# Kernel tuning notes

Measured on AMD Instinct MI355X. Metric: run time of the kernel, lower is better.

The kernel has to match this reference:

```python
import jax, jax.numpy as jnp
import numpy as np

B, S, D_MODEL = 2, 2048, 2048
H, DS, DG, DV = 16, 64, 64, 128
ROPE_BASE = 10000.0
NEG_INF = -1e9


def _rope(x, base=ROPE_BASE):
    # x: [B, S, H, D] -> rotate-half RoPE over positions 0..S-1
    d = x.shape[-1]
    half = d // 2
    inv_freq = 1.0 / (base ** (jnp.arange(half, dtype=jnp.float32) / half))
    ang = jnp.arange(x.shape[1], dtype=jnp.float32)[:, None] * inv_freq  # [S, half]
    cos = jnp.cos(ang)[None, :, None, :]
    sin = jnp.sin(ang)[None, :, None, :]
    x1, x2 = x[..., :half], x[..., half:]
    return jnp.concatenate([x1 * cos - x2 * sin, x1 * sin + x2 * cos], axis=-1)


def setup_inputs() -> dict:
    key = jax.random.key(0)
    ks = jax.random.split(key, 8)
    s = lambda fan_in: 1.0 / np.sqrt(fan_in)
    return {
        "x": jax.random.normal(ks[0], (B, S, D_MODEL), dtype=jnp.float32),
        "wq_sem": jax.random.normal(ks[1], (D_MODEL, H * DS), dtype=jnp.float32) * s(D_MODEL),
        "wk_sem": jax.random.normal(ks[2], (D_MODEL, H * DS), dtype=jnp.float32) * s(D_MODEL),
        "wq_geo": jax.random.normal(ks[3], (D_MODEL, H * DG), dtype=jnp.float32) * s(D_MODEL),
        "wk_geo": jax.random.normal(ks[4], (D_MODEL, H * DG), dtype=jnp.float32) * s(D_MODEL),
        "wv": jax.random.normal(ks[5], (D_MODEL, H * DV), dtype=jnp.float32) * s(D_MODEL),
        "wo": jax.random.normal(ks[6], (H * DV, D_MODEL), dtype=jnp.float32) * s(H * DV),
        "gate_logit": jax.random.normal(ks[7], (H,), dtype=jnp.float32),
    }


def reference(x, wq_sem, wk_sem, wq_geo, wk_geo, wv, wo, gate_logit):
    b, sl, _ = x.shape
    # Projections -> [B, S, H, d]
    qs = (x @ wq_sem).reshape(b, sl, H, DS)
    ksem = (x @ wk_sem).reshape(b, sl, H, DS)
    qg = _rope((x @ wq_geo).reshape(b, sl, H, DG))
    kg = _rope((x @ wk_geo).reshape(b, sl, H, DG))
    v = (x @ wv).reshape(b, sl, H, DV)

    sem_scale = 1.0 / np.sqrt(DS)
    geo_scale = 1.0 / np.sqrt(DG)
    sem_scores = jnp.einsum("bqhd,bkhd->bhqk", qs, ksem) * sem_scale
    geo_scores = jnp.einsum("bqhd,bkhd->bhqk", qg, kg) * geo_scale

    # Learned per-head gate mixing semantic vs geometric paths
    g = jax.nn.sigmoid(gate_logit)[None, :, None, None]
    scores = g * sem_scores + (1.0 - g) * geo_scores

    causal = jnp.tril(jnp.ones((sl, sl), dtype=bool))
    scores = jnp.where(causal[None, None], scores, NEG_INF)
    attn = jax.nn.softmax(scores, axis=-1)

    out = jnp.einsum("bhqk,bkhd->bqhd", attn, v).reshape(b, sl, H * DV)
    return out @ wo
```

## Files before the change

kernel.cpp:

```cpp
#include <hip/hip_runtime.h>
#include <hip/hip_bf16.h>

typedef unsigned short u16;
typedef __attribute__((ext_vector_type(4))) float floatx4;
typedef __attribute__((ext_vector_type(8))) __bf16 bf16x8;

__device__ __forceinline__ u16 f2bf(float f) {
  unsigned int x = __builtin_bit_cast(unsigned int, f);
  unsigned int r = (x + 0x7fffu + ((x >> 16) & 1u)) >> 16;
  return (u16)r;
}
__device__ __forceinline__ float bf2f(u16 u) {
  unsigned int x = ((unsigned int)u) << 16;
  return __builtin_bit_cast(float, x);
}
__device__ __forceinline__ floatx4 mfma16(bf16x8 a, bf16x8 b, floatx4 c) {
  return __builtin_amdgcn_mfma_f32_16x16x32_bf16(a, b, c, 0, 0, 0);
}
__device__ __forceinline__ void gload16(const u16* g, u16* l) {
  __builtin_amdgcn_global_load_lds(
      (const __attribute__((address_space(1))) unsigned int*)g,
      (__attribute__((address_space(3))) unsigned int*)l, 16, 0, 0);
}
#define SCHEDB() __builtin_amdgcn_sched_barrier(0)
#define SBAR() __builtin_amdgcn_s_barrier()

#define BB 2
#define SS 2048
#define DM 2048
#define HH 16
#define PCOLS 6144

__global__ void convert_bf16_k(const float* __restrict__ src, u16* __restrict__ dst, size_t n) {
  size_t i = ((size_t)blockIdx.x * blockDim.x + threadIdx.x) * 4;
  if (i + 3 >= n) { for (size_t j = i; j < n; ++j) dst[j] = f2bf(src[j]); return; }
  float4 v = *(const float4*)&src[i];
  ushort4 o; o.x = f2bf(v.x); o.y = f2bf(v.y); o.z = f2bf(v.z); o.w = f2bf(v.w);
  *(ushort4*)&dst[i] = o;
}

__global__ void transpose_all_k(const float* w0, const float* w1, const float* w2,
                                const float* w3, const float* w4, const float* w5,
                                u16* __restrict__ WcatT, u16* __restrict__ WoT) {
  __shared__ float tile[32][33];
  const int z = blockIdx.z;
  const float* src; u16* dst; int cols;
  if (z == 0)      { src = w0; dst = WcatT;                        cols = 1024; }
  else if (z == 1) { src = w1; dst = WcatT + (size_t)1024 * 2048;  cols = 1024; }
  else if (z == 2) { src = w2; dst = WcatT + (size_t)2048 * 2048;  cols = 1024; }
  else if (z == 3) { src = w3; dst = WcatT + (size_t)3072 * 2048;  cols = 1024; }
  else if (z == 4) { src = w4; dst = WcatT + (size_t)4096 * 2048;  cols = 2048; }
  else             { src = w5; dst = WoT;                          cols = 2048; }
  int c0 = blockIdx.x * 32;
  if (c0 >= cols) return;
  int r0 = blockIdx.y * 32;
  int tx = threadIdx.x, ty = threadIdx.y;
#pragma unroll
  for (int i = 0; i < 4; ++i)
    tile[ty + i * 8][tx] = src[(size_t)(r0 + ty + i * 8) * cols + c0 + tx];
  __syncthreads();
#pragma unroll
  for (int i = 0; i < 4; ++i)
    dst[(size_t)(c0 + ty + i * 8) * 2048 + r0 + tx] = f2bf(tile[tx][ty + i * 8]);
}

__global__ void vtrans_k(const u16* __restrict__ P, u16* __restrict__ VtG) {
  __shared__ u16 t[32][33];
  int b = blockIdx.z;
  int c0 = blockIdx.x * 32;
  int s0 = blockIdx.y * 32;
  int tx = threadIdx.x, ty = threadIdx.y;
#pragma unroll
  for (int i = 0; i < 4; ++i)
    t[ty + i * 8][tx] = P[((size_t)b * SS + s0 + ty + i * 8) * PCOLS + 4096 + c0 + tx];
  __syncthreads();
#pragma unroll
  for (int i = 0; i < 4; ++i)
    VtG[((size_t)b * 2048 + c0 + ty + i * 8) * SS + s0 + tx] = t[tx][ty + i * 8];
}

__global__ void rope_table_k(float* __restrict__ cosT, float* __restrict__ sinT) {
  int idx = blockIdx.x * 256 + threadIdx.x;
  int s = idx >> 5, d = idx & 31;
  double inv = pow(10000.0, -(double)d / 32.0);
  double ang = (double)s * inv;
  cosT[idx] = (float)cos(ang);
  sinT[idx] = (float)sin(ang);
}

__global__ void rope_apply_k(u16* __restrict__ P, const float* __restrict__ cosT,
                             const float* __restrict__ sinT) {
  int idx = blockIdx.x * 256 + threadIdx.x;
  int d = idx & 31, h = (idx >> 5) & 15, reg = (idx >> 9) & 1, row = idx >> 10;
  int s = row & (SS - 1);
  size_t base = (size_t)row * PCOLS + (reg ? 3072 : 2048) + h * 64 + d;
  float x1 = bf2f(P[base]), x2 = bf2f(P[base + 32]);
  float c = cosT[s * 32 + d], sn = sinT[s * 32 + d];
  P[base] = f2bf(x1 * c - x2 * sn);
  P[base + 32] = f2bf(x1 * sn + x2 * c);
}

template <int NFB, bool OUTF32>
__global__ __launch_bounds__(256, 1)
void gemm4_k(const u16* __restrict__ A, const u16* __restrict__ Bt,
             void* __restrict__ Cout, int M, int N, int K) {
  constexpr int BH = NFB / 2;
  __shared__ alignas(16) u16 lds[16384 + NFB * 8192];
  const int tid = threadIdx.x;
  const int wid = tid >> 6, lane = tid & 63;
  const int lr = lane & 15, lg = lane >> 4;
  const int m0 = blockIdx.y * 128, n0 = blockIdx.x * (NFB * 64);
  const int NT = K >> 6;
  const int NSLAB = NT * 4;

  const int aoff = lr * 32 + ((lg ^ ((lr >> 1) & 3)) * 8);

  const int srow = wid * 16 + (lane >> 2);
  const int sgl = (((lane & 3) ^ ((lane >> 3) & 3)) * 8);
  const u16* Asrc = A + (size_t)(m0 + srow) * K + sgl;
  const u16* Bsrc = Bt + (size_t)(n0 + srow) * K + sgl;

  floatx4 acc[8][NFB];
#pragma unroll
  for (int m = 0; m < 8; ++m)
#pragma unroll
    for (int n = 0; n < NFB; ++n) acc[m][n] = (floatx4){0.f, 0.f, 0.f, 0.f};

  auto stgA = [&](int tile, int kh) {
    u16* d = lds + ((tile & 1) * 2 + kh) * 4096 + wid * 512;
    const u16* s = Asrc + tile * 64 + kh * 32;
#pragma unroll
    for (int c = 0; c < 2; ++c) gload16(s + (size_t)(c * 64) * K, d + c * 2048);
  };
  auto stgB = [&](int tile, int kh) {
    u16* d = lds + 16384 + ((tile & 1) * 2 + kh) * (NFB * 2048) + wid * 512;
    const u16* s = Bsrc + tile * 64 + kh * 32;
#pragma unroll
    for (int c = 0; c < NFB; ++c) gload16(s + (size_t)(c * 64) * K, d + c * 2048);
  };
  auto stage_slab = [&](int s) {
    if (s >= NSLAB) return;
    int tile = s >> 2, kind = s & 3;
    if (kind == 0) stgA(tile, 0);
    else if (kind == 1) stgB(tile, 0);
    else if (kind == 2) stgA(tile, 1);
    else stgB(tile, 1);
  };

  for (int s = 0; s < 7; ++s) stage_slab(s);
  if constexpr (NFB == 6) asm volatile("s_waitcnt vmcnt(10)" ::: "memory");
  else                    asm volatile("s_waitcnt vmcnt(8)" ::: "memory");
  SCHEDB(); SBAR(); SCHEDB();

  bf16x8 af[8], bfv[BH];

#pragma unroll 1
  for (int it = 0; it < (NT >> 1); ++it) {
    const int t = it * 2;
    const int sb = t * 4 + 6;
    const bool more = (t + 2 < NT);

#define PH(BUF, KK, NH, SL, DOVM)                                               \
    {                                                                           \
      const u16* Ab = lds + ((BUF) * 2 + (KK)) * 4096;                          \
      const u16* Bb = lds + 16384 + ((BUF) * 2 + (KK)) * (NFB * 2048);          \
      if ((NH) == 0) {                                                          \
        _Pragma("unroll") for (int m = 0; m < 8; ++m)                           \
          af[m] = *(const bf16x8*)&Ab[(m * 16) * 32 + aoff];                    \
      }                                                                         \
      _Pragma("unroll") for (int j = 0; j < BH; ++j)                            \
        bfv[j] = *(const bf16x8*)&Bb[(wid * NFB * 16 + ((NH) * BH + j) * 16) * 32 + aoff]; \
      stage_slab(sb + (SL));                                                    \
      SCHEDB(); SBAR(); SCHEDB();                                               \
      __builtin_amdgcn_s_setprio(1);                                            \
      _Pragma("unroll") for (int m = 0; m < 8; ++m)                             \
        _Pragma("unroll") for (int j = 0; j < BH; ++j)                          \
          acc[m][(NH) * BH + j] = mfma16(af[m], bfv[j], acc[m][(NH) * BH + j]); \
      __builtin_amdgcn_s_setprio(0);                                            \
      if (DOVM) {                                                               \
        if (more) {                                                             \
          if constexpr (NFB == 6) asm volatile("s_waitcnt vmcnt(10)" ::: "memory"); \
          else                    asm volatile("s_waitcnt vmcnt(8)" ::: "memory");  \
        } else {                                                                \
          asm volatile("s_waitcnt vmcnt(0)" ::: "memory");                      \
        }                                                                       \
      }                                                                         \
      SCHEDB(); SBAR(); SCHEDB();                                               \
    }

    PH(0, 0, 0, 1, 0)
    PH(0, 0, 1, 2, 0)
    PH(0, 1, 0, 3, 0)
    PH(0, 1, 1, 4, 1)
    PH(1, 0, 0, 5, 0)
    PH(1, 0, 1, 6, 0)
    PH(1, 1, 0, 7, 0)
    PH(1, 1, 1, 8, 1)
#undef PH
  }

#pragma unroll
  for (int m = 0; m < 8; ++m) {
    int row0 = m0 + m * 16 + lg * 4;
#pragma unroll
    for (int n = 0; n < NFB; ++n) {
      int col = n0 + wid * NFB * 16 + n * 16 + lr;
#pragma unroll
      for (int r = 0; r < 4; ++r) {
        size_t off = (size_t)(row0 + r) * N + col;
        if (OUTF32) ((float*)Cout)[off] = acc[m][n][r];
        else        ((u16*)Cout)[off] = f2bf(acc[m][n][r]);
      }
    }
  }
}

__device__ __forceinline__ bf16x8 load_scaled(const u16* p, float s) {
  uint4 raw = *(const uint4*)p;
  const u16* ru = (const u16*)&raw;
  bf16x8 out;
#pragma unroll
  for (int j = 0; j < 8; ++j) out[j] = (__bf16)(bf2f(ru[j]) * s);
  return out;
}

__global__ __launch_bounds__(256, 3)
void attn_k(const u16* __restrict__ P, const u16* __restrict__ VtG,
            const float* __restrict__ gate, u16* __restrict__ AttO) {
  const int pairi = blockIdx.x >> 4;
  const int h = blockIdx.x & 15;
  const int b = blockIdx.y;
  const int tid = threadIdx.x, wid = tid >> 6, lane = tid & 63;
  const int lr = lane & 15, lg = lane >> 4;
  const size_t rowb = (size_t)b * SS;

  const float g = 1.f / (1.f + __expf(-gate[h]));
  const float ssc = g * 0.125f;
  const float gsc = (1.f - g) * 0.125f;

  __shared__ alignas(16) u16 Ks[64 * 64];
  __shared__ alignas(16) u16 Kg[64 * 64];
  __shared__ alignas(16) u16 Vt[128 * 64];
  __shared__ alignas(16) u16 Pw[4][16 * 64];

  const int strow = tid >> 3;
  const int stg = ((tid & 7) ^ (strow & 7)) * 8;
  const int swz = lr & 7;

  for (int half = 0; half < 2; ++half) {
    const int qb = half ? (31 - pairi) : pairi;
    const int q0 = qb * 64;

    const u16* qbase = P + (rowb + q0 + wid * 16 + lr) * PCOLS + h * 64;
    bf16x8 qs[2], qg[2];
#pragma unroll
    for (int kk = 0; kk < 2; ++kk) {
      qs[kk] = load_scaled(qbase + kk * 32 + lg * 8, ssc);
      qg[kk] = load_scaled(qbase + 2048 + kk * 32 + lg * 8, gsc);
    }

    float m_r = -1e30f, l_r = 0.f;
    floatx4 o[8];
#pragma unroll
    for (int n = 0; n < 8; ++n) o[n] = (floatx4){0.f, 0.f, 0.f, 0.f};

    const int nkv = q0 + 64;
    for (int kv0 = 0; kv0 < nkv; kv0 += 64) {
      __syncthreads();
      {
        const u16* ks = P + (rowb + kv0 + strow) * PCOLS + 1024 + h * 64 + stg;
        const u16* gs = P + (rowb + kv0 + strow) * PCOLS + 3072 + h * 64 + stg;
        gload16(ks, Ks + wid * 512);
        gload16(gs, Kg + wid * 512);
        gload16(ks + (size_t)32 * PCOLS, Ks + 2048 + wid * 512);
        gload16(gs + (size_t)32 * PCOLS, Kg + 2048 + wid * 512);
      }
      {
        const u16* vs = VtG + ((size_t)b * 2048 + h * 128 + strow) * SS + kv0 + stg;
#pragma unroll
        for (int c = 0; c < 4; ++c)
          gload16(vs + (size_t)(c * 32) * SS, Vt + c * 2048 + wid * 512);
      }
      __syncthreads();

      floatx4 sc[4];
#pragma unroll
      for (int s = 0; s < 4; ++s) sc[s] = (floatx4){0.f, 0.f, 0.f, 0.f};
#pragma unroll
      for (int kk = 0; kk < 2; ++kk) {
#pragma unroll
        for (int s = 0; s < 4; ++s) {
          bf16x8 kf = *(const bf16x8*)&Ks[(s * 16 + lr) * 64 + ((kk * 4 + lg) ^ swz) * 8];
          bf16x8 gf = *(const bf16x8*)&Kg[(s * 16 + lr) * 64 + ((kk * 4 + lg) ^ swz) * 8];
          sc[s] = mfma16(kf, qs[kk], sc[s]);
          sc[s] = mfma16(gf, qg[kk], sc[s]);
        }
      }

      const int qrow = q0 + wid * 16 + lr;
      const bool needmask = (kv0 + 63 > q0 + wid * 16);
      float vv[4][4];
      float vmax = -1e30f;
#pragma unroll
      for (int s = 0; s < 4; ++s)
#pragma unroll
        for (int r = 0; r < 4; ++r) {
          float val = sc[s][r];
          if (needmask) val = (kv0 + s * 16 + lg * 4 + r <= qrow) ? val : -1e30f;
          vv[s][r] = val;
          vmax = fmaxf(vmax, val);
        }
      vmax = fmaxf(vmax, __shfl_xor(vmax, 16));
      vmax = fmaxf(vmax, __shfl_xor(vmax, 32));
      float mnew = fmaxf(m_r, vmax);
      float corr = __expf(m_r - mnew);
      float psum = 0.f;
#pragma unroll
      for (int s = 0; s < 4; ++s)
#pragma unroll
        for (int r = 0; r < 4; ++r) {
          vv[s][r] = __expf(vv[s][r] - mnew);
          psum += vv[s][r];
        }
      psum += __shfl_xor(psum, 16);
      psum += __shfl_xor(psum, 32);
      l_r = l_r * corr + psum;
      m_r = mnew;

#pragma unroll
      for (int s = 0; s < 4; ++s)
#pragma unroll
        for (int t = 0; t < 2; ++t) {
          unsigned int w;
          asm("v_cvt_pk_bf16_f32 %0, %1, %2" : "=v"(w) : "v"(vv[s][2 * t]), "v"(vv[s][2 * t + 1]));
          int u16off = lr * 64 + ((s * 2 + (lg >> 1)) ^ swz) * 8 + (lg & 1) * 4 + t * 2;
          *(unsigned int*)&Pw[wid][u16off] = w;
        }

      float crr[4];
#pragma unroll
      for (int r = 0; r < 4; ++r) crr[r] = __shfl(corr, lg * 4 + r);
#pragma unroll
      for (int n = 0; n < 8; ++n)
#pragma unroll
        for (int r = 0; r < 4; ++r) o[n][r] *= crr[r];

      asm volatile("s_waitcnt lgkmcnt(0)" ::: "memory");
      SCHEDB();
      bf16x8 pa0 = *(const bf16x8*)&Pw[wid][lr * 64 + (lg ^ swz) * 8];
      bf16x8 pa1 = *(const bf16x8*)&Pw[wid][lr * 64 + ((4 + lg) ^ swz) * 8];
#pragma unroll
      for (int n = 0; n < 8; ++n) {
        bf16x8 vb0 = *(const bf16x8*)&Vt[(n * 16 + lr) * 64 + (lg ^ swz) * 8];
        bf16x8 vb1 = *(const bf16x8*)&Vt[(n * 16 + lr) * 64 + ((4 + lg) ^ swz) * 8];
        o[n] = mfma16(pa0, vb0, o[n]);
        o[n] = mfma16(pa1, vb1, o[n]);
      }
    }

    float linv = 1.f / l_r;
    float lnv[4];
#pragma unroll
    for (int r = 0; r < 4; ++r) lnv[r] = __shfl(linv, lg * 4 + r);
#pragma unroll
    for (int n = 0; n < 8; ++n)
#pragma unroll
      for (int r = 0; r < 4; ++r) {
        float val = o[n][r] * lnv[r];
        AttO[(rowb + q0 + wid * 16 + lg * 4 + r) * (size_t)(HH * 128) + h * 128 + n * 16 + lr] =
            f2bf(val);
      }
  }
}

extern "C" void kernel_launch(void* const* d_in, const int* in_sizes, int n_in,
                              void* d_out, int out_size, void* d_ws, size_t ws_size,
                              hipStream_t stream) {
  const float* x       = (const float*)d_in[0];
  const float* wq_sem  = (const float*)d_in[1];
  const float* wk_sem  = (const float*)d_in[2];
  const float* wq_geo  = (const float*)d_in[3];
  const float* wk_geo  = (const float*)d_in[4];
  const float* wv      = (const float*)d_in[5];
  const float* wo      = (const float*)d_in[6];
  const float* gate    = (const float*)d_in[7];

  char* ws = (char*)d_ws;
  u16* Xbf   = (u16*)(ws);
  u16* WcatT = (u16*)(ws + 16777216);
  u16* WoT   = (u16*)(ws + 16777216 + 25165824);
  u16* P     = (u16*)(ws + 16777216 + 25165824 + 8388608);
  float* cosT = (float*)(ws + 16777216 + 25165824 + 8388608 + 50331648);
  float* sinT = cosT + 2048 * 32;
  u16* AttO = Xbf;
  u16* VtG  = WcatT;

  dim3 tb(32, 8);
  convert_bf16_k<<<8192, 256, 0, stream>>>(x, Xbf, (size_t)4096 * 2048);
  transpose_all_k<<<dim3(64, 64, 6), tb, 0, stream>>>(wq_sem, wk_sem, wq_geo, wk_geo,
                                                      wv, wo, WcatT, WoT);
  rope_table_k<<<256, 256, 0, stream>>>(cosT, sinT);

  gemm4_k<6, false><<<dim3(16, 32), 256, 0, stream>>>(Xbf, WcatT, P, 4096, 6144, 2048);
  rope_apply_k<<<16384, 256, 0, stream>>>(P, cosT, sinT);
  vtrans_k<<<dim3(64, 64, 2), tb, 0, stream>>>(P, VtG);
  attn_k<<<dim3(256, 2), 256, 0, stream>>>(P, VtG, gate, AttO);
  gemm4_k<4, true><<<dim3(8, 32), 256, 0, stream>>>(AttO, WoT, d_out, 4096, 2048, 2048);
}
```

Measured before the change: 266.0 us.

## Double-buffer K tiles in LDS and load V directly into registers

The K/Kg tiles are now double-buffered in shared memory, and the next tile is prefetched while the current one is being computed, with explicit vmcnt waits in place of a load-then-sync pattern. The V tile is no longer staged through LDS. Each wave reads its V fragments straight from global memory into registers before the QK work, so the latency is hidden behind the softmax. This trims LDS traffic and one barrier per iteration. In exchange it uses many more VGPRs (16 bf16x8 values), which risks lower occupancy, and each wave makes redundant global reads of V.

```diff
diff --git a/kernel.cpp b/kernel.cpp
--- a/kernel.cpp
+++ b/kernel.cpp
@@ -238,14 +238,15 @@
   const float ssc = g * 0.125f;
   const float gsc = (1.f - g) * 0.125f;
 
-  __shared__ alignas(16) u16 Ks[64 * 64];
-  __shared__ alignas(16) u16 Kg[64 * 64];
-  __shared__ alignas(16) u16 Vt[128 * 64];
+  __shared__ alignas(16) u16 Ks[2][64 * 64];
+  __shared__ alignas(16) u16 Kg[2][64 * 64];
   __shared__ alignas(16) u16 Pw[4][16 * 64];
 
   const int strow = tid >> 3;
   const int stg = ((tid & 7) ^ (strow & 7)) * 8;
   const int swz = lr & 7;
+
+  const u16* vbase0 = VtG + ((size_t)b * 2048 + h * 128 + lr) * SS + lg * 8;
 
   for (int half = 0; half < 2; ++half) {
     const int qb = half ? (31 - pairi) : pairi;
@@ -265,23 +266,35 @@
     for (int n = 0; n < 8; ++n) o[n] = (floatx4){0.f, 0.f, 0.f, 0.f};
 
     const int nkv = q0 + 64;
+
+    auto stageK = [&](int kv0, int buf) {
+      const u16* ks = P + (rowb + kv0 + strow) * PCOLS + 1024 + h * 64 + stg;
+      const u16* gs = P + (rowb + kv0 + strow) * PCOLS + 3072 + h * 64 + stg;
+      gload16(ks, &Ks[buf][wid * 512]);
+      gload16(gs, &Kg[buf][wid * 512]);
+      gload16(ks + (size_t)32 * PCOLS, &Ks[buf][2048 + wid * 512]);
+      gload16(gs + (size_t)32 * PCOLS, &Kg[buf][2048 + wid * 512]);
+    };
+
+    stageK(0, 0);
+
     for (int kv0 = 0; kv0 < nkv; kv0 += 64) {
-      __syncthreads();
-      {
-        const u16* ks = P + (rowb + kv0 + strow) * PCOLS + 1024 + h * 64 + stg;
-        const u16* gs = P + (rowb + kv0 + strow) * PCOLS + 3072 + h * 64 + stg;
-        gload16(ks, Ks + wid * 512);
-        gload16(gs, Kg + wid * 512);
-        gload16(ks + (size_t)32 * PCOLS, Ks + 2048 + wid * 512);
-        gload16(gs + (size_t)32 * PCOLS, Kg + 2048 + wid * 512);
+      const int cur = (kv0 >> 6) & 1;
+      const bool more = (kv0 + 64 < nkv);
+
+      bf16x8 vr[16];
+      const u16* vb_ = vbase0 + kv0;
+#pragma unroll
+      for (int n = 0; n < 8; ++n) {
+        vr[n * 2]     = *(const bf16x8*)(vb_ + (size_t)(n * 16) * SS);
+        vr[n * 2 + 1] = *(const bf16x8*)(vb_ + (size_t)(n * 16) * SS + 32);
       }
-      {
-        const u16* vs = VtG + ((size_t)b * 2048 + h * 128 + strow) * SS + kv0 + stg;
-#pragma unroll
-        for (int c = 0; c < 4; ++c)
-          gload16(vs + (size_t)(c * 32) * SS, Vt + c * 2048 + wid * 512);
-      }
-      __syncthreads();
+      SCHEDB();
+      if (more) stageK(kv0 + 64, cur ^ 1);
+      SCHEDB();
+      if (more) asm volatile("s_waitcnt vmcnt(20)" ::: "memory");
+      else      asm volatile("s_waitcnt vmcnt(16)" ::: "memory");
+      SCHEDB(); SBAR(); SCHEDB();
 
       floatx4 sc[4];
 #pragma unroll
@@ -290,8 +303,8 @@
       for (int kk = 0; kk < 2; ++kk) {
 #pragma unroll
         for (int s = 0; s < 4; ++s) {
-          bf16x8 kf = *(const bf16x8*)&Ks[(s * 16 + lr) * 64 + ((kk * 4 + lg) ^ swz) * 8];
-          bf16x8 gf = *(const bf16x8*)&Kg[(s * 16 + lr) * 64 + ((kk * 4 + lg) ^ swz) * 8];
+          bf16x8 kf = *(const bf16x8*)&Ks[cur][(s * 16 + lr) * 64 + ((kk * 4 + lg) ^ swz) * 8];
+          bf16x8 gf = *(const bf16x8*)&Kg[cur][(s * 16 + lr) * 64 + ((kk * 4 + lg) ^ swz) * 8];
           sc[s] = mfma16(kf, qs[kk], sc[s]);
           sc[s] = mfma16(gf, qg[kk], sc[s]);
         }
@@ -345,17 +358,20 @@
 #pragma unroll
         for (int r = 0; r < 4; ++r) o[n][r] *= crr[r];
 
+      SCHEDB();
+      if (more) asm volatile("s_waitcnt vmcnt(4)" ::: "memory");
+      else      asm volatile("s_waitcnt vmcnt(0)" ::: "memory");
+      SCHEDB();
       asm volatile("s_waitcnt lgkmcnt(0)" ::: "memory");
       SCHEDB();
       bf16x8 pa0 = *(const bf16x8*)&Pw[wid][lr * 64 + (lg ^ swz) * 8];
       bf16x8 pa1 = *(const bf16x8*)&Pw[wid][lr * 64 + ((4 + lg) ^ swz) * 8];
 #pragma unroll
       for (int n = 0; n < 8; ++n) {
-        bf16x8 vb0 = *(const bf16x8*)&Vt[(n * 16 + lr) * 64 + (lg ^ swz) * 8];
-        bf16x8 vb1 = *(const bf16x8*)&Vt[(n * 16 + lr) * 64 + ((4 + lg) ^ swz) * 8];
-        o[n] = mfma16(pa0, vb0, o[n]);
-        o[n] = mfma16(pa1, vb1, o[n]);
+        o[n] = mfma16(pa0, vr[n * 2], o[n]);
+        o[n] = mfma16(pa1, vr[n * 2 + 1], o[n]);
       }
+      SCHEDB(); SBAR(); SCHEDB();
     }
 
     float linv = 1.f / l_r;
```

New measurement: 334.8 us. 25.9% more time.
